# Performance work log

Hardware: AMD Instinct MI355X
Metric: run time of the kernel (lower is better)

The kernel has to match this reference:

```python
import jax, jax.numpy as jnp
import numpy as np

EPS = 1e-07


def setup_inputs() -> dict:
    key = jax.random.key(0)
    k_emb, k_a, k_b, k_r = jax.random.split(key, 4)
    B, F, N = 8, 6, 2048
    # momentum channel (index 4) must be strictly positive for log()
    emb = jax.random.uniform(k_emb, (B, F, N), dtype=jnp.float32, minval=0.1, maxval=1.0)
    # parameters: base_value * (rand*0.02 + 0.99), as in the torch __init__
    alpha = 1.0 * (jax.random.uniform(k_a, (1, 1), dtype=jnp.float32) * 0.02 + 0.99)
    beta = 1.0 * (jax.random.uniform(k_b, (1, 1, 1), dtype=jnp.float32) * 0.02 + 0.99)
    radius = 0.5 * (jax.random.uniform(k_r, (1, 1, 1), dtype=jnp.float32) * 0.02 + 0.99)
    return {"emb": emb, "alpha": alpha, "beta": beta, "radius": radius}


def reference(emb, alpha, beta, radius):
    # emb: (B, F, N); coords are channels 1:3, momentum is channel 4
    coord = emb[:, 1:3, :]                                  # (B, 2, N)
    sqnorm = jnp.sum(coord * coord, axis=1)                 # (B, N)
    dotprod = jnp.einsum('bcn,bcm->bnm', coord, coord)      # (B, N, N)
    sqdist = sqnorm[:, :, None] + sqnorm[:, None, :] - 2.0 * dotprod
    sqradius = radius ** 2 + EPS                            # (1,1,1) broadcasts
    sqdist = sqdist / sqradius

    momentum = emb[:, 4, :]                                 # (B, N)
    pow_momenta = jnp.exp(2.0 * alpha * jnp.log(momentum))  # (B, N)
    # pairwise min (the _mmin expand/stack/min dance, fused)
    min_momenta = jnp.minimum(pow_momenta[:, :, None], pow_momenta[:, None, :])
    d_ij_alpha = sqdist * min_momenta                       # (B, N, N)

    d_min = jnp.min(pow_momenta, axis=1, keepdims=True)[:, :, None] + EPS  # (B,1,1)
    d_ij_center = (d_ij_alpha - d_min) / d_min
    d_ij_center = d_ij_center / 10000.0
    d_ij_norm = (beta ** 2) * d_ij_center
    w_ij = jnp.exp(-d_ij_norm)                              # (B, N, N)
    return w_ij
```

## Files before the change

kernel.cpp:

```cpp
#include <hip/hip_runtime.h>

#define EPS 1e-7f
#define BATCH 8
#define NPT 2048
#define NFEAT 6

#define WS_POW   0
#define WS_DMIN  (BATCH * NPT)
#define WS_ISR   (BATCH * NPT + BATCH)
#define WS_BEFF  (BATCH * NPT + BATCH + 1)

__global__ __launch_bounds__(256)
void precompute_kernel(const float* __restrict__ emb,
                       const float* __restrict__ alpha,
                       const float* __restrict__ beta,
                       const float* __restrict__ radius,
                       float* __restrict__ ws) {
    int b = blockIdx.x;
    int tid = threadIdx.x;
    float a2 = 2.0f * alpha[0];
    const float* mom = emb + (size_t)b * NFEAT * NPT + 4 * NPT;
    float* powp = ws + WS_POW + (size_t)b * NPT;

    float local_min = 3.0e38f;
    for (int n = tid; n < NPT; n += 256) {
        float m = mom[n];
        float p = __expf(a2 * __logf(m));
        powp[n] = p;
        local_min = fminf(local_min, p);
    }
    for (int off = 32; off > 0; off >>= 1)
        local_min = fminf(local_min, __shfl_down(local_min, off, 64));
    __shared__ float smin[4];
    int wave = tid >> 6;
    if ((tid & 63) == 0) smin[wave] = local_min;
    __syncthreads();
    if (tid == 0) {
        float m = fminf(fminf(smin[0], smin[1]), fminf(smin[2], smin[3]));
        ws[WS_DMIN + b] = m + EPS;
    }
    if (b == 0 && tid == 0) {
        float r = radius[0];
        ws[WS_ISR] = 1.0f / (r * r + EPS);
        float bt = beta[0];
        ws[WS_BEFF] = bt * bt * 1e-4f;
    }
}

__global__ __launch_bounds__(512)
void wij_kernel(const float* __restrict__ emb,
                const float* __restrict__ ws,
                float* __restrict__ out) {
    int row = blockIdx.x;
    int b = row >> 11;
    int n = row & (NPT - 1);

    const float* base = emb + (size_t)b * NFEAT * NPT;
    float xn = base[1 * NPT + n];
    float yn = base[2 * NPT + n];
    const float* powp = ws + WS_POW + (size_t)b * NPT;
    float pn   = powp[n];
    float dmin = ws[WS_DMIN + b];
    float isr  = ws[WS_ISR];
    float beff = ws[WS_BEFF];
    float c = beff / dmin;
    float cisr = c * isr;

    int t = threadIdx.x;
    float4 cx = ((const float4*)(base + 1 * NPT))[t];
    float4 cy = ((const float4*)(base + 2 * NPT))[t];
    float4 pw = ((const float4*)powp)[t];

    float4 w;
    {
        float dx = xn - cx.x, dy = yn - cy.x;
        float da = (dx * dx + dy * dy) * fminf(pn, pw.x);
        w.x = __expf(beff - cisr * da);
    }
    {
        float dx = xn - cx.y, dy = yn - cy.y;
        float da = (dx * dx + dy * dy) * fminf(pn, pw.y);
        w.y = __expf(beff - cisr * da);
    }
    {
        float dx = xn - cx.z, dy = yn - cy.z;
        float da = (dx * dx + dy * dy) * fminf(pn, pw.z);
        w.z = __expf(beff - cisr * da);
    }
    {
        float dx = xn - cx.w, dy = yn - cy.w;
        float da = (dx * dx + dy * dy) * fminf(pn, pw.w);
        w.w = __expf(beff - cisr * da);
    }

    float* outrow = out + (size_t)row * NPT;
    ((float4*)outrow)[t] = w;
}

extern "C" void kernel_launch(void* const* d_in, const int* in_sizes, int n_in,
                              void* d_out, int out_size, void* d_ws, size_t ws_size,
                              hipStream_t stream) {
    const float* emb    = (const float*)d_in[0];
    const float* alpha  = (const float*)d_in[1];
    const float* beta   = (const float*)d_in[2];
    const float* radius = (const float*)d_in[3];
    float* out = (float*)d_out;
    float* ws  = (float*)d_ws;

    precompute_kernel<<<BATCH, 256, 0, stream>>>(emb, alpha, beta, radius, ws);
    wij_kernel<<<BATCH * NPT, 512, 0, stream>>>(emb, ws, out);
}
```

Before: 149.1 us.

## Process eight rows per block with nontemporal stores and exp2 constant folding

Each block now computes eight output rows instead of one, so the column coordinate and power vectors are loaded once and reused across the eight rows. Output writes use nontemporal stores to avoid polluting cache with the large streamed output. The scale constants are folded into one per-batch coefficient including log2(e) so the inner loop uses the hardware exp2 directly. This cuts the grid by eight, which reduces parallelism per block but should still fill the device.

New measurement: 152.5 us. +2.3%, slower.

```diff
diff --git a/kernel.cpp b/kernel.cpp
--- a/kernel.cpp
+++ b/kernel.cpp
@@ -4,11 +4,13 @@
 #define BATCH 8
 #define NPT 2048
 #define NFEAT 6
+#define LOG2E 1.44269504088896340736f
+
+typedef float vf4 __attribute__((ext_vector_type(4)));
 
 #define WS_POW   0
-#define WS_DMIN  (BATCH * NPT)
-#define WS_ISR   (BATCH * NPT + BATCH)
-#define WS_BEFF  (BATCH * NPT + BATCH + 1)
+#define WS_CB    (BATCH * NPT)
+#define WS_BEFF2 (BATCH * NPT + BATCH)
 
 __global__ __launch_bounds__(256)
 void precompute_kernel(const float* __restrict__ emb,
@@ -36,65 +38,68 @@
     if ((tid & 63) == 0) smin[wave] = local_min;
     __syncthreads();
     if (tid == 0) {
-        float m = fminf(fminf(smin[0], smin[1]), fminf(smin[2], smin[3]));
-        ws[WS_DMIN + b] = m + EPS;
-    }
-    if (b == 0 && tid == 0) {
-        float r = radius[0];
-        ws[WS_ISR] = 1.0f / (r * r + EPS);
+        float dmin = fminf(fminf(smin[0], smin[1]), fminf(smin[2], smin[3])) + EPS;
+        float r  = radius[0];
         float bt = beta[0];
-        ws[WS_BEFF] = bt * bt * 1e-4f;
+        float beff2 = bt * bt * 1e-4f * LOG2E;
+        ws[WS_CB + b] = beff2 / (dmin * (r * r + EPS));
+        if (b == 0) ws[WS_BEFF2] = beff2;
     }
 }
 
+#define RPB 8
 __global__ __launch_bounds__(512)
 void wij_kernel(const float* __restrict__ emb,
                 const float* __restrict__ ws,
                 float* __restrict__ out) {
-    int row = blockIdx.x;
-    int b = row >> 11;
-    int n = row & (NPT - 1);
+    int blk = blockIdx.x;
+    int b  = blk / (NPT / RPB);
+    int n0 = (blk % (NPT / RPB)) * RPB;
 
     const float* base = emb + (size_t)b * NFEAT * NPT;
-    float xn = base[1 * NPT + n];
-    float yn = base[2 * NPT + n];
     const float* powp = ws + WS_POW + (size_t)b * NPT;
-    float pn   = powp[n];
-    float dmin = ws[WS_DMIN + b];
-    float isr  = ws[WS_ISR];
-    float beff = ws[WS_BEFF];
-    float c = beff / dmin;
-    float cisr = c * isr;
+    float cb    = ws[WS_CB + b];
+    float beff2 = ws[WS_BEFF2];
 
     int t = threadIdx.x;
-    float4 cx = ((const float4*)(base + 1 * NPT))[t];
-    float4 cy = ((const float4*)(base + 2 * NPT))[t];
-    float4 pw = ((const float4*)powp)[t];
+    vf4 cx = ((const vf4*)(base + 1 * NPT))[t];
+    vf4 cy = ((const vf4*)(base + 2 * NPT))[t];
+    vf4 pw = ((const vf4*)powp)[t];
 
-    float4 w;
-    {
-        float dx = xn - cx.x, dy = yn - cy.x;
-        float da = (dx * dx + dy * dy) * fminf(pn, pw.x);
-        w.x = __expf(beff - cisr * da);
-    }
-    {
-        float dx = xn - cx.y, dy = yn - cy.y;
-        float da = (dx * dx + dy * dy) * fminf(pn, pw.y);
-        w.y = __expf(beff - cisr * da);
-    }
-    {
-        float dx = xn - cx.z, dy = yn - cy.z;
-        float da = (dx * dx + dy * dy) * fminf(pn, pw.z);
-        w.z = __expf(beff - cisr * da);
-    }
-    {
-        float dx = xn - cx.w, dy = yn - cy.w;
-        float da = (dx * dx + dy * dy) * fminf(pn, pw.w);
-        w.w = __expf(beff - cisr * da);
+    float xn[RPB], yn[RPB], pn[RPB];
+    #pragma unroll
+    for (int r = 0; r < RPB; ++r) {
+        xn[r] = base[1 * NPT + n0 + r];
+        yn[r] = base[2 * NPT + n0 + r];
+        pn[r] = powp[n0 + r];
     }
 
-    float* outrow = out + (size_t)row * NPT;
-    ((float4*)outrow)[t] = w;
+    vf4* outp = (vf4*)(out + (size_t)(b * NPT + n0) * NPT) + t;
+    #pragma unroll
+    for (int r = 0; r < RPB; ++r) {
+        vf4 w;
+        {
+            float dx = xn[r] - cx.x, dy = yn[r] - cy.x;
+            float da = (dx * dx + dy * dy) * fminf(pn[r], pw.x);
+            w.x = __builtin_amdgcn_exp2f(beff2 - cb * da);
+        }
+        {
+            float dx = xn[r] - cx.y, dy = yn[r] - cy.y;
+            float da = (dx * dx + dy * dy) * fminf(pn[r], pw.y);
+            w.y = __builtin_amdgcn_exp2f(beff2 - cb * da);
+        }
+        {
+            float dx = xn[r] - cx.z, dy = yn[r] - cy.z;
+            float da = (dx * dx + dy * dy) * fminf(pn[r], pw.z);
+            w.z = __builtin_amdgcn_exp2f(beff2 - cb * da);
+        }
+        {
+            float dx = xn[r] - cx.w, dy = yn[r] - cy.w;
+            float da = (dx * dx + dy * dy) * fminf(pn[r], pw.w);
+            w.w = __builtin_amdgcn_exp2f(beff2 - cb * da);
+        }
+        __builtin_nontemporal_store(w, outp + (size_t)r * (NPT / 4));
+    }
 }
 
 extern "C" void kernel_launch(void* const* d_in, const int* in_sizes, int n_in,
@@ -108,5 +113,5 @@
     float* ws  = (float*)d_ws;
 
     precompute_kernel<<<BATCH, 256, 0, stream>>>(emb, alpha, beta, radius, ws);
-    wij_kernel<<<BATCH * NPT, 512, 0, stream>>>(emb, ws, out);
+    wij_kernel<<<(BATCH * NPT) / RPB, 512, 0, stream>>>(emb, ws, out);
 }
```
